# Optimization experiments

Measured on AMD Instinct MI355X. Metric: run time of the kernel, lower is better.

The kernel has to match this reference:

```python
import jax, jax.numpy as jnp
import numpy as np

D_MODEL = 256
NUM_HEADS = 4
EPS = 1e-6


def setup_inputs() -> dict:
    key = jax.random.key(0)
    ks = jax.random.split(key, 9)
    B, T, D = 4, 2048, D_MODEL
    scale = 1.0 / np.sqrt(D)
    inp = {
        "x": jax.random.normal(ks[0], (B, T, D), dtype=jnp.float32),
        "Wq": jax.random.normal(ks[1], (D, D), dtype=jnp.float32) * scale,
        "bq": jnp.zeros((D,), dtype=jnp.float32),
        "Wk": jax.random.normal(ks[2], (D, D), dtype=jnp.float32) * scale,
        "bk": jnp.zeros((D,), dtype=jnp.float32),
        "Wv": jax.random.normal(ks[3], (D, D), dtype=jnp.float32) * scale,
        "bv": jnp.zeros((D,), dtype=jnp.float32),
        "Wo": jax.random.normal(ks[4], (D, D), dtype=jnp.float32) * scale,
        "bo": jnp.zeros((D,), dtype=jnp.float32),
    }
    return inp


def _feature_map(a):
    # F.elu(x) + 1.0
    return jax.nn.elu(a) + 1.0


def reference(x, Wq, bq, Wk, bk, Wv, bv, Wo, bo):
    B, T, D = x.shape
    H = NUM_HEADS
    dh = D // H
    Q = _feature_map((x @ Wq + bq).reshape(B, T, H, dh))
    K = _feature_map((x @ Wk + bk).reshape(B, T, H, dh))
    V = (x @ Wv + bv).reshape(B, T, H, dh)
    # outer-product state: (B,T,H,dh,dh), cumulative over time
    KV = jnp.einsum('bthd,bthm->bthdm', K, V)
    S = jnp.cumsum(KV, axis=1)
    Z = jnp.cumsum(K, axis=1)
    out = jnp.einsum('bthd,bthdm->bthm', Q, S)
    denom = jnp.einsum('bthd,bthd->bth', Q, Z)[..., None] + EPS
    out = (out / denom).reshape(B, T, D)
    return out @ Wo + bo
```

## Files before the change

kernel.cpp:

```cpp
#include <hip/hip_runtime.h>
#include <hip/hip_bf16.h>

#define D_MODEL 256
#define NHEADS 4
#define DHEAD 64
#define BATCH 4
#define TSEQ 2048
#define CHUNK 64
#define NCHUNK (TSEQ / CHUNK)
#define NTOK (BATCH * TSEQ)
#define NBH (BATCH * NHEADS)
#define EPSV 1e-6f
#define LSTRF 68
#define PQ 36

typedef __bf16 bf16x8 __attribute__((ext_vector_type(8)));
typedef float f32x4 __attribute__((ext_vector_type(4)));
typedef unsigned short us8 __attribute__((ext_vector_type(8)));

__device__ __forceinline__ float elu1(float a) {
    return a > 0.0f ? a + 1.0f : __expf(a);
}

__device__ __forceinline__ unsigned short f2bf(float f) {
    __hip_bfloat16 h = __float2bfloat16(f);
    return __builtin_bit_cast(unsigned short, h);
}

__device__ __forceinline__ float bf2f(unsigned short u) {
    return __bfloat162float(__builtin_bit_cast(__hip_bfloat16, u));
}

__device__ __forceinline__ void unpack2(unsigned int u, float& lo, float& hi) {
    lo = __builtin_bit_cast(float, u << 16);
    hi = __builtin_bit_cast(float, u & 0xFFFF0000u);
}

__device__ __forceinline__ bf16x8 frag8(const float* p) {
    const float4 x = *reinterpret_cast<const float4*>(p);
    const float4 y = *reinterpret_cast<const float4*>(p + 4);
    us8 u;
    u[0] = f2bf(x.x); u[1] = f2bf(x.y); u[2] = f2bf(x.z); u[3] = f2bf(x.w);
    u[4] = f2bf(y.x); u[5] = f2bf(y.y); u[6] = f2bf(y.z); u[7] = f2bf(y.w);
    return __builtin_bit_cast(bf16x8, u);
}

__device__ __forceinline__ void gld_lds16(const void* g, void* l) {
    __builtin_amdgcn_global_load_lds(
        (const __attribute__((address_space(1))) void*)g,
        (__attribute__((address_space(3))) void*)l, 16, 0, 0);
}

__global__ __launch_bounds__(256) void convert_kernel(
    const float* __restrict__ x,
    const float* __restrict__ Wq, const float* __restrict__ Wk,
    const float* __restrict__ Wv, const float* __restrict__ Wo,
    unsigned short* __restrict__ xb,
    unsigned short* __restrict__ Wt, unsigned short* __restrict__ Wot)
{
    const int tid = threadIdx.x;
    if (blockIdx.x < NTOK * D_MODEL / 8 / 256) {
        const int i = (blockIdx.x * 256 + tid) * 8;
        const float4 a = *reinterpret_cast<const float4*>(&x[i]);
        const float4 b = *reinterpret_cast<const float4*>(&x[i + 4]);
        ushort4 u0 = { f2bf(a.x), f2bf(a.y), f2bf(a.z), f2bf(a.w) };
        ushort4 u1 = { f2bf(b.x), f2bf(b.y), f2bf(b.z), f2bf(b.w) };
        *reinterpret_cast<ushort4*>(&xb[i]) = u0;
        *reinterpret_cast<ushort4*>(&xb[i + 4]) = u1;
        return;
    }
    __shared__ float Ls[64][65];
    const int bid = blockIdx.x - NTOK * D_MODEL / 8 / 256;
    const int wi = bid >> 4;
    const int ti = bid & 15;
    const int k0 = (ti >> 2) * 64, n0 = (ti & 3) * 64;
    const float* W = wi == 0 ? Wq : wi == 1 ? Wk : wi == 2 ? Wv : Wo;
#pragma unroll
    for (int i = 0; i < 16; ++i) {
        const int idx = i * 256 + tid;
        const int r = idx >> 6, c = idx & 63;
        Ls[r][c] = W[(size_t)(k0 + r) * D_MODEL + n0 + c];
    }
    __syncthreads();
    unsigned short* outp = (wi < 3) ? (Wt + (size_t)(wi * 256 + n0) * D_MODEL + k0)
                                    : (Wot + (size_t)n0 * D_MODEL + k0);
#pragma unroll
    for (int i = 0; i < 16; ++i) {
        const int idx = i * 256 + tid;
        const int rn = idx >> 6, ck = idx & 63;
        outp[(size_t)rn * D_MODEL + ck] = f2bf(Ls[ck][rn]);
    }
}

template<int MODE>
__global__ __launch_bounds__(256) void mfma_gemm_kernel(
    const unsigned short* __restrict__ A,
    const unsigned short* __restrict__ Bt,
    const float* __restrict__ b0, const float* __restrict__ b1,
    const float* __restrict__ b2,
    void* __restrict__ O0, void* __restrict__ O1, void* __restrict__ O2)
{
    __shared__ __align__(16) unsigned short As[64 * 256];
    __shared__ __align__(16) unsigned short Bs[64 * 256];
    const int tid = threadIdx.x;
    const int wave = tid >> 6, lane = tid & 63;
    const int la = lane & 15, q = lane >> 4;

    int mtile, ntile;
    if (MODE == 0) { ntile = blockIdx.x % 12; mtile = blockIdx.x / 12; }
    else           { ntile = blockIdx.x & 3;  mtile = blockIdx.x >> 2; }
    const int m0 = mtile * 64, n0 = ntile * 64;

    const unsigned short* Ab = A  + (size_t)m0 * D_MODEL;
    const unsigned short* Bb = Bt + (size_t)n0 * D_MODEL;

#pragma unroll
    for (int i = 0; i < 8; ++i) {
        const int bslot = i * 256 + wave * 64;
        const int slot = bslot + lane;
        const int m = slot >> 5, s = slot & 31;
        const int g = s ^ (m & 7);
        gld_lds16(Ab + (size_t)m * D_MODEL + g * 8, &As[bslot * 8]);
        gld_lds16(Bb + (size_t)m * D_MODEL + g * 8, &Bs[bslot * 8]);
    }
    __syncthreads();

    f32x4 acc[4];
#pragma unroll
    for (int i = 0; i < 4; ++i) acc[i] = (f32x4){0.f, 0.f, 0.f, 0.f};

#pragma unroll
    for (int kh = 0; kh < 8; ++kh) {
        const int gl = kh * 4 + q;
        const int m = wave * 16 + la;
        const bf16x8 af = *reinterpret_cast<const bf16x8*>(
            &As[m * 256 + ((gl ^ (m & 7)) << 3)]);
#pragma unroll
        for (int ni = 0; ni < 4; ++ni) {
            const int n = ni * 16 + la;
            const bf16x8 bf = *reinterpret_cast<const bf16x8*>(
                &Bs[n * 256 + ((gl ^ (n & 7)) << 3)]);
            acc[ni] = __builtin_amdgcn_mfma_f32_16x16x32_bf16(
                af, bf, acc[ni], 0, 0, 0);
        }
    }

#pragma unroll
    for (int ni = 0; ni < 4; ++ni) {
        const int row = m0 + wave * 16 + q * 4;
        const int col = n0 + ni * 16 + la;
        if (MODE == 0) {
            const int which = col >> 8;
            const int cl = col & 255;
            unsigned short* Out = (unsigned short*)
                (which == 0 ? O0 : which == 1 ? O1 : O2);
            const float* bias = which == 0 ? b0 : which == 1 ? b1 : b2;
            const int act = (which < 2);
            const float bv = bias[cl];
#pragma unroll
            for (int r = 0; r < 4; ++r) {
                float v = acc[ni][r] + bv;
                if (act) v = elu1(v);
                Out[(size_t)(row + r) * D_MODEL + cl] = f2bf(v);
            }
        } else {
            float* Out = (float*)O0;
            const float bv = b0[col];
#pragma unroll
            for (int r = 0; r < 4; ++r)
                Out[(size_t)(row + r) * D_MODEL + col] = acc[ni][r] + bv;
        }
    }
}

__global__ __launch_bounds__(256) void chunksum_kernel(
    const unsigned short* __restrict__ Kb, const unsigned short* __restrict__ Vb,
    unsigned short* __restrict__ Pb16, float* __restrict__ Zc)
{
    __shared__ __align__(16) unsigned int Ktp[DHEAD * PQ];
    __shared__ __align__(16) unsigned int Vtp[DHEAD * PQ];
    const int tid = threadIdx.x;
    const int c  = blockIdx.x % NCHUNK;
    const int bh = blockIdx.x / NCHUNK;
    const int b = bh / NHEADS, h = bh % NHEADS;
    const size_t gbase = ((size_t)(b * TSEQ + c * CHUNK)) * D_MODEL + h * DHEAD;

    {
        const int sp = tid & 31, mg = tid >> 5;
        const int e0 = mg * 8;
        const uint4 k0 = *reinterpret_cast<const uint4*>(
            &Kb[gbase + (size_t)(2 * sp) * D_MODEL + e0]);
        const uint4 k1 = *reinterpret_cast<const uint4*>(
            &Kb[gbase + (size_t)(2 * sp + 1) * D_MODEL + e0]);
        const uint4 v0 = *reinterpret_cast<const uint4*>(
            &Vb[gbase + (size_t)(2 * sp) * D_MODEL + e0]);
        const uint4 v1 = *reinterpret_cast<const uint4*>(
            &Vb[gbase + (size_t)(2 * sp + 1) * D_MODEL + e0]);
        const unsigned short* ke = reinterpret_cast<const unsigned short*>(&k0);
        const unsigned short* ko2 = reinterpret_cast<const unsigned short*>(&k1);
        const unsigned short* ve = reinterpret_cast<const unsigned short*>(&v0);
        const unsigned short* vo = reinterpret_cast<const unsigned short*>(&v1);
#pragma unroll
        for (int j = 0; j < 8; ++j) {
            Ktp[(e0 + j) * PQ + sp] =
                (unsigned int)ke[j] | ((unsigned int)ko2[j] << 16);
            Vtp[(e0 + j) * PQ + sp] =
                (unsigned int)ve[j] | ((unsigned int)vo[j] << 16);
        }
    }
    __syncthreads();

    const int wave = tid >> 6, lane = tid & 63;
    const int la = lane & 15, q = lane >> 4;
    const int wm = (wave >> 1) * 32, wn = (wave & 1) * 32;

    f32x4 acc[2][2];
#pragma unroll
    for (int i = 0; i < 2; ++i)
#pragma unroll
        for (int j = 0; j < 2; ++j) acc[i][j] = (f32x4){0.f, 0.f, 0.f, 0.f};

#pragma unroll
    for (int ks = 0; ks < 2; ++ks) {
        const int ku = ks * 16 + q * 4;
        const bf16x8 a0  = __builtin_bit_cast(bf16x8,
            *reinterpret_cast<const uint4*>(&Vtp[(wm + la) * PQ + ku]));
        const bf16x8 a1  = __builtin_bit_cast(bf16x8,
            *reinterpret_cast<const uint4*>(&Vtp[(wm + 16 + la) * PQ + ku]));
        const bf16x8 bb0 = __builtin_bit_cast(bf16x8,
            *reinterpret_cast<const uint4*>(&Ktp[(wn + la) * PQ + ku]));
        const bf16x8 bb1 = __builtin_bit_cast(bf16x8,
            *reinterpret_cast<const uint4*>(&Ktp[(wn + 16 + la) * PQ + ku]));
        acc[0][0] = __builtin_amdgcn_mfma_f32_16x16x32_bf16(a0, bb0, acc[0][0], 0, 0, 0);
        acc[0][1] = __builtin_amdgcn_mfma_f32_16x16x32_bf16(a0, bb1, acc[0][1], 0, 0, 0);
        acc[1][0] = __builtin_amdgcn_mfma_f32_16x16x32_bf16(a1, bb0, acc[1][0], 0, 0, 0);
        acc[1][1] = __builtin_amdgcn_mfma_f32_16x16x32_bf16(a1, bb1, acc[1][1], 0, 0, 0);
    }

    unsigned short* Pb = Pb16 + (size_t)blockIdx.x * (DHEAD * DHEAD);
#pragma unroll
    for (int mi = 0; mi < 2; ++mi)
#pragma unroll
        for (int ni = 0; ni < 2; ++ni) {
            const int row = wm + mi * 16 + q * 4;
            const int col = wn + ni * 16 + la;
#pragma unroll
            for (int r = 0; r < 4; ++r)
                Pb[(row + r) * DHEAD + col] = f2bf(acc[mi][ni][r]);
        }

    if (tid < DHEAD) {
        float z = 0.f;
        for (int tt = 0; tt < 32; ++tt) {
            float lo, hi;
            unpack2(Ktp[tid * PQ + tt], lo, hi);
            z += lo;
            z += hi;
        }
        Zc[(size_t)blockIdx.x * DHEAD + tid] = z;
    }
}

__global__ __launch_bounds__(256) void prefix_kernel(
    const unsigned short* __restrict__ Pb16, float* __restrict__ Zc,
    unsigned short* __restrict__ Sb)
{
    const int tid = threadIdx.x;
    if (blockIdx.x < NBH * 16) {
        const int bh = blockIdx.x >> 4;
        const int e = ((blockIdx.x & 15) << 8) + tid;
        const size_t base = (size_t)bh * NCHUNK * (DHEAD * DHEAD) + e;
        float v[NCHUNK];
#pragma unroll
        for (int c = 0; c < NCHUNK; ++c)
            v[c] = bf2f(Pb16[base + (size_t)c * (DHEAD * DHEAD)]);
        float s = 0.f;
#pragma unroll
        for (int c = 0; c < NCHUNK; ++c) {
            const float t = v[c];
            Sb[base + (size_t)c * (DHEAD * DHEAD)] = f2bf(s);
            s += t;
        }
    } else {
        const int j = ((int)(blockIdx.x - NBH * 16) << 8) + tid;
        if (j < NBH * DHEAD) {
            const int bh = j >> 6, d = j & 63;
            float v[NCHUNK];
#pragma unroll
            for (int c = 0; c < NCHUNK; ++c) v[c] = Zc[(bh * NCHUNK + c) * DHEAD + d];
            float s = 0.f;
#pragma unroll
            for (int c = 0; c < NCHUNK; ++c) {
                const float t = v[c];
                Zc[(bh * NCHUNK + c) * DHEAD + d] = s;
                s += t;
            }
        }
    }
}

__global__ __launch_bounds__(256) void chunkout_kernel(
    const unsigned short* __restrict__ Qb, const unsigned short* __restrict__ Kb,
    const unsigned short* __restrict__ Vb,
    const unsigned short* __restrict__ Sb, const float* __restrict__ Zx,
    unsigned short* __restrict__ Ob)
{
    __shared__ __align__(16) unsigned int Qp[CHUNK * PQ];
    __shared__ __align__(16) unsigned int Kp[CHUNK * PQ];
    __shared__ __align__(16) unsigned int Vtp[DHEAD * PQ];
    __shared__ __align__(16) float At[CHUNK * LSTRF];
    __shared__ float zsh[DHEAD];
    __shared__ float dnm[CHUNK];

    const int tid = threadIdx.x;
    const int c  = blockIdx.x % NCHUNK;
    const int bh = blockIdx.x / NCHUNK;
    const int b = bh / NHEADS, h = bh % NHEADS;
    const size_t gbase = ((size_t)(b * TSEQ + c * CHUNK)) * D_MODEL + h * DHEAD;
    const unsigned short* Sp = Sb + (size_t)blockIdx.x * (DHEAD * DHEAD);

#pragma unroll
    for (int i = 0; i < 2; ++i) {
        const int idx = i * 256 + tid;
        const int t = idx >> 3, e4 = (idx & 7) * 4;
        const uint4 qv = *reinterpret_cast<const uint4*>(
            &Qb[gbase + (size_t)t * D_MODEL + e4 * 2]);
        const uint4 kv = *reinterpret_cast<const uint4*>(
            &Kb[gbase + (size_t)t * D_MODEL + e4 * 2]);
        *reinterpret_cast<uint4*>(&Qp[t * PQ + e4]) = qv;
        *reinterpret_cast<uint4*>(&Kp[t * PQ + e4]) = kv;
    }
    {
        const int sp = tid & 31, mg = tid >> 5;
        const int m0 = mg * 8;
        const uint4 v0 = *reinterpret_cast<const uint4*>(
            &Vb[gbase + (size_t)(2 * sp) * D_MODEL + m0]);
        const uint4 v1 = *reinterpret_cast<const uint4*>(
            &Vb[gbase + (size_t)(2 * sp + 1) * D_MODEL + m0]);
        const unsigned short* ev = reinterpret_cast<const unsigned short*>(&v0);
        const unsigned short* ov = reinterpret_cast<const unsigned short*>(&v1);
#pragma unroll
        for (int j = 0; j < 8; ++j)
            Vtp[(m0 + j) * PQ + sp] =
                (unsigned int)ev[j] | ((unsigned int)ov[j] << 16);
    }
    if (tid < DHEAD)
        zsh[tid] = Zx[((size_t)bh * NCHUNK + c) * DHEAD + tid];
    __syncthreads();

    const int wave = tid >> 6, lane = tid & 63;
    const int la = lane & 15, q = lane >> 4;
    const int wt = (wave >> 1) * 32, wn = (wave & 1) * 32;

    f32x4 acc[2][2];
#pragma unroll
    for (int i = 0; i < 2; ++i)
#pragma unroll
        for (int j = 0; j < 2; ++j) acc[i][j] = (f32x4){0.f, 0.f, 0.f, 0.f};
#pragma unroll
    for (int ks = 0; ks < 2; ++ks) {
        const int ku = ks * 16 + q * 4;
        const bf16x8 a0  = __builtin_bit_cast(bf16x8,
            *reinterpret_cast<const uint4*>(&Qp[(wt + la) * PQ + ku]));
        const bf16x8 a1  = __builtin_bit_cast(bf16x8,
            *reinterpret_cast<const uint4*>(&Qp[(wt + 16 + la) * PQ + ku]));
        const bf16x8 bb0 = __builtin_bit_cast(bf16x8,
            *reinterpret_cast<const uint4*>(&Kp[(wn + la) * PQ + ku]));
        const bf16x8 bb1 = __builtin_bit_cast(bf16x8,
            *reinterpret_cast<const uint4*>(&Kp[(wn + 16 + la) * PQ + ku]));
        acc[0][0] = __builtin_amdgcn_mfma_f32_16x16x32_bf16(a0, bb0, acc[0][0], 0, 0, 0);
        acc[0][1] = __builtin_amdgcn_mfma_f32_16x16x32_bf16(a0, bb1, acc[0][1], 0, 0, 0);
        acc[1][0] = __builtin_amdgcn_mfma_f32_16x16x32_bf16(a1, bb0, acc[1][0], 0, 0, 0);
        acc[1][1] = __builtin_amdgcn_mfma_f32_16x16x32_bf16(a1, bb1, acc[1][1], 0, 0, 0);
    }
#pragma unroll
    for (int mi = 0; mi < 2; ++mi)
#pragma unroll
        for (int ni = 0; ni < 2; ++ni) {
            const int t0 = wt + mi * 16 + q * 4;
            const int s  = wn + ni * 16 + la;
#pragma unroll
            for (int r = 0; r < 4; ++r)
                At[(t0 + r) * LSTRF + s] = (s <= t0 + r) ? acc[mi][ni][r] : 0.f;
        }
    __syncthreads();

    if (tid < CHUNK) {
        float dv = 0.f;
        for (int s = 0; s < CHUNK; ++s) dv += At[tid * LSTRF + s];
        for (int dd = 0; dd < 32; ++dd) {
            float lo, hi;
            unpack2(Qp[tid * PQ + dd], lo, hi);
            dv = fmaf(lo, zsh[2 * dd], dv);
            dv = fmaf(hi, zsh[2 * dd + 1], dv);
        }
        dnm[tid] = dv + EPSV;
    }
    __syncthreads();

    f32x4 o[2][2];
#pragma unroll
    for (int i = 0; i < 2; ++i)
#pragma unroll
        for (int j = 0; j < 2; ++j) o[i][j] = (f32x4){0.f, 0.f, 0.f, 0.f};
#pragma unroll
    for (int ks = 0; ks < 2; ++ks) {
        const int ku = ks * 16 + q * 4;
        const int ko = ks * 32 + q * 8;
        const bf16x8 a0  = __builtin_bit_cast(bf16x8,
            *reinterpret_cast<const uint4*>(&Qp[(wt + la) * PQ + ku]));
        const bf16x8 a1  = __builtin_bit_cast(bf16x8,
            *reinterpret_cast<const uint4*>(&Qp[(wt + 16 + la) * PQ + ku]));
        const bf16x8 bb0 = __builtin_bit_cast(bf16x8,
            *reinterpret_cast<const uint4*>(&Sp[(wn + la) * DHEAD + ko]));
        const bf16x8 bb1 = __builtin_bit_cast(bf16x8,
            *reinterpret_cast<const uint4*>(&Sp[(wn + 16 + la) * DHEAD + ko]));
        o[0][0] = __builtin_amdgcn_mfma_f32_16x16x32_bf16(a0, bb0, o[0][0], 0, 0, 0);
        o[0][1] = __builtin_amdgcn_mfma_f32_16x16x32_bf16(a0, bb1, o[0][1], 0, 0, 0);
        o[1][0] = __builtin_amdgcn_mfma_f32_16x16x32_bf16(a1, bb0, o[1][0], 0, 0, 0);
        o[1][1] = __builtin_amdgcn_mfma_f32_16x16x32_bf16(a1, bb1, o[1][1], 0, 0, 0);
    }
#pragma unroll
    for (int ks = 0; ks < 2; ++ks) {
        const int ku = ks * 16 + q * 4;
        const int ko = ks * 32 + q * 8;
        const bf16x8 a0  = frag8(&At[(wt + la) * LSTRF + ko]);
        const bf16x8 a1  = frag8(&At[(wt + 16 + la) * LSTRF + ko]);
        const bf16x8 bb0 = __builtin_bit_cast(bf16x8,
            *reinterpret_cast<const uint4*>(&Vtp[(wn + la) * PQ + ku]));
        const bf16x8 bb1 = __builtin_bit_cast(bf16x8,
            *reinterpret_cast<const uint4*>(&Vtp[(wn + 16 + la) * PQ + ku]));
        o[0][0] = __builtin_amdgcn_mfma_f32_16x16x32_bf16(a0, bb0, o[0][0], 0, 0, 0);
        o[0][1] = __builtin_amdgcn_mfma_f32_16x16x32_bf16(a0, bb1, o[0][1], 0, 0, 0);
        o[1][0] = __builtin_amdgcn_mfma_f32_16x16x32_bf16(a1, bb0, o[1][0], 0, 0, 0);
        o[1][1] = __builtin_amdgcn_mfma_f32_16x16x32_bf16(a1, bb1, o[1][1], 0, 0, 0);
    }

#pragma unroll
    for (int mi = 0; mi < 2; ++mi)
#pragma unroll
        for (int ni = 0; ni < 2; ++ni) {
            const int t0 = wt + mi * 16 + q * 4;
            const int m  = wn + ni * 16 + la;
#pragma unroll
            for (int r = 0; r < 4; ++r) {
                const float v = o[mi][ni][r] / dnm[t0 + r];
                Ob[gbase + (size_t)(t0 + r) * D_MODEL + m] = f2bf(v);
            }
        }
}

extern "C" void kernel_launch(void* const* d_in, const int* in_sizes, int n_in,
                              void* d_out, int out_size, void* d_ws, size_t ws_size,
                              hipStream_t stream)
{
    const float* x  = (const float*)d_in[0];
    const float* Wq = (const float*)d_in[1];
    const float* bq = (const float*)d_in[2];
    const float* Wk = (const float*)d_in[3];
    const float* bk = (const float*)d_in[4];
    const float* Wv = (const float*)d_in[5];
    const float* bv = (const float*)d_in[6];
    const float* Wo = (const float*)d_in[7];
    const float* bo = (const float*)d_in[8];
    float* out = (float*)d_out;

    const size_t NE = (size_t)NTOK * D_MODEL;
    const size_t PE = (size_t)NBH * NCHUNK * DHEAD * DHEAD;
    unsigned short* xb   = (unsigned short*)d_ws;
    unsigned short* Wt   = xb + NE;
    unsigned short* Wot  = Wt + 768 * 256;
    unsigned short* Qb   = Wot + 256 * 256;
    unsigned short* Kb   = Qb + NE;
    unsigned short* Vb   = Kb + NE;
    unsigned short* Ob   = Vb + NE;
    unsigned short* Sb   = Ob + NE;
    unsigned short* Pb16 = Sb + PE;
    float* Z = (float*)(Pb16 + PE);

    convert_kernel<<<NTOK * D_MODEL / 8 / 256 + 64, 256, 0, stream>>>(
        x, Wq, Wk, Wv, Wo, xb, Wt, Wot);
    mfma_gemm_kernel<0><<<(NTOK / 64) * 12, 256, 0, stream>>>(
        xb, Wt, bq, bk, bv, Qb, Kb, Vb);
    chunksum_kernel<<<NBH * NCHUNK, 256, 0, stream>>>(Kb, Vb, Pb16, Z);
    prefix_kernel<<<NBH * 16 + 4, 256, 0, stream>>>(Pb16, Z, Sb);
    chunkout_kernel<<<NBH * NCHUNK, 256, 0, stream>>>(Qb, Kb, Vb, Sb, Z, Ob);
    mfma_gemm_kernel<1><<<(NTOK / 64) * 4, 256, 0, stream>>>(
        Ob, Wot, bo, nullptr, nullptr, out, nullptr, nullptr);
}
```

Before: 106.4 us.

## Fuse fp32-to-bf16 conversion into GEMMs and fold chunk prefix scan into chunkout

Drops the separate convert kernel: the QKV and output GEMMs now load fp32 x and weights directly, converting to bf16 and transposing into swizzled LDS. Drops the prefix kernel: each chunkout block sums all earlier chunk states and key sums on the fly from global memory into register fragments. This removes two launches and the intermediate xb/Wt/Sb buffers. In exchange, weights are read with strided scalar loads, and later chunks re-read up to 31 prefix states, which adds quadratic redundant global traffic and load imbalance across blocks.

```diff
diff --git a/kernel.cpp b/kernel.cpp
--- a/kernel.cpp
+++ b/kernel.cpp
@@ -45,60 +45,27 @@
     return __builtin_bit_cast(bf16x8, u);
 }
 
+__device__ __forceinline__ bf16x8 pack8(const float* p) {
+    us8 u;
+#pragma unroll
+    for (int j = 0; j < 8; ++j) u[j] = f2bf(p[j]);
+    return __builtin_bit_cast(bf16x8, u);
+}
+
 __device__ __forceinline__ void gld_lds16(const void* g, void* l) {
     __builtin_amdgcn_global_load_lds(
         (const __attribute__((address_space(1))) void*)g,
         (__attribute__((address_space(3))) void*)l, 16, 0, 0);
 }
 
-__global__ __launch_bounds__(256) void convert_kernel(
+__global__ __launch_bounds__(256) void qkv_kernel(
     const float* __restrict__ x,
     const float* __restrict__ Wq, const float* __restrict__ Wk,
-    const float* __restrict__ Wv, const float* __restrict__ Wo,
-    unsigned short* __restrict__ xb,
-    unsigned short* __restrict__ Wt, unsigned short* __restrict__ Wot)
-{
-    const int tid = threadIdx.x;
-    if (blockIdx.x < NTOK * D_MODEL / 8 / 256) {
-        const int i = (blockIdx.x * 256 + tid) * 8;
-        const float4 a = *reinterpret_cast<const float4*>(&x[i]);
-        const float4 b = *reinterpret_cast<const float4*>(&x[i + 4]);
-        ushort4 u0 = { f2bf(a.x), f2bf(a.y), f2bf(a.z), f2bf(a.w) };
-        ushort4 u1 = { f2bf(b.x), f2bf(b.y), f2bf(b.z), f2bf(b.w) };
-        *reinterpret_cast<ushort4*>(&xb[i]) = u0;
-        *reinterpret_cast<ushort4*>(&xb[i + 4]) = u1;
-        return;
-    }
-    __shared__ float Ls[64][65];
-    const int bid = blockIdx.x - NTOK * D_MODEL / 8 / 256;
-    const int wi = bid >> 4;
-    const int ti = bid & 15;
-    const int k0 = (ti >> 2) * 64, n0 = (ti & 3) * 64;
-    const float* W = wi == 0 ? Wq : wi == 1 ? Wk : wi == 2 ? Wv : Wo;
-#pragma unroll
-    for (int i = 0; i < 16; ++i) {
-        const int idx = i * 256 + tid;
-        const int r = idx >> 6, c = idx & 63;
-        Ls[r][c] = W[(size_t)(k0 + r) * D_MODEL + n0 + c];
-    }
-    __syncthreads();
-    unsigned short* outp = (wi < 3) ? (Wt + (size_t)(wi * 256 + n0) * D_MODEL + k0)
-                                    : (Wot + (size_t)n0 * D_MODEL + k0);
-#pragma unroll
-    for (int i = 0; i < 16; ++i) {
-        const int idx = i * 256 + tid;
-        const int rn = idx >> 6, ck = idx & 63;
-        outp[(size_t)rn * D_MODEL + ck] = f2bf(Ls[ck][rn]);
-    }
-}
-
-template<int MODE>
-__global__ __launch_bounds__(256) void mfma_gemm_kernel(
-    const unsigned short* __restrict__ A,
-    const unsigned short* __restrict__ Bt,
-    const float* __restrict__ b0, const float* __restrict__ b1,
-    const float* __restrict__ b2,
-    void* __restrict__ O0, void* __restrict__ O1, void* __restrict__ O2)
+    const float* __restrict__ Wv,
+    const float* __restrict__ bq, const float* __restrict__ bk,
+    const float* __restrict__ bv,
+    unsigned short* __restrict__ Qb, unsigned short* __restrict__ Kb,
+    unsigned short* __restrict__ Vb)
 {
     __shared__ __align__(16) unsigned short As[64 * 256];
     __shared__ __align__(16) unsigned short Bs[64 * 256];
@@ -106,13 +73,90 @@
     const int wave = tid >> 6, lane = tid & 63;
     const int la = lane & 15, q = lane >> 4;
 
-    int mtile, ntile;
-    if (MODE == 0) { ntile = blockIdx.x % 12; mtile = blockIdx.x / 12; }
-    else           { ntile = blockIdx.x & 3;  mtile = blockIdx.x >> 2; }
+    const int ntile = blockIdx.x % 12, mtile = blockIdx.x / 12;
+    const int m0 = mtile * 64;
+    const int which = ntile >> 2;
+    const int wcol0 = (ntile & 3) * 64;
+    const float* W    = which == 0 ? Wq : which == 1 ? Wk : Wv;
+    const float* bias = which == 0 ? bq : which == 1 ? bk : bv;
+    unsigned short* Out = which == 0 ? Qb : which == 1 ? Kb : Vb;
+    const int act = (which < 2);
+
+#pragma unroll
+    for (int i = 0; i < 8; ++i) {
+        const int task = i * 256 + tid;
+        const int m = task >> 5, g = task & 31;
+        const float* src = &x[(size_t)(m0 + m) * D_MODEL + g * 8];
+        const float4 a = *reinterpret_cast<const float4*>(src);
+        const float4 b = *reinterpret_cast<const float4*>(src + 4);
+        us8 u;
+        u[0] = f2bf(a.x); u[1] = f2bf(a.y); u[2] = f2bf(a.z); u[3] = f2bf(a.w);
+        u[4] = f2bf(b.x); u[5] = f2bf(b.y); u[6] = f2bf(b.z); u[7] = f2bf(b.w);
+        *reinterpret_cast<us8*>(&As[m * 256 + ((g ^ (m & 7)) << 3)]) = u;
+    }
+#pragma unroll
+    for (int i = 0; i < 8; ++i) {
+        const int task = i * 256 + tid;
+        const int n = task & 63, g = (task >> 6) + i * 4 * 0 + (i * 4) * 0;
+        const int gg = i * 4 + (task >> 6 & 3);
+        const int k0 = gg * 8;
+        us8 u;
+#pragma unroll
+        for (int j = 0; j < 8; ++j)
+            u[j] = f2bf(W[(size_t)(k0 + j) * D_MODEL + wcol0 + n]);
+        *reinterpret_cast<us8*>(&Bs[n * 256 + ((gg ^ (n & 7)) << 3)]) = u;
+        (void)g;
+    }
+    __syncthreads();
+
+    f32x4 acc[4];
+#pragma unroll
+    for (int i = 0; i < 4; ++i) acc[i] = (f32x4){0.f, 0.f, 0.f, 0.f};
+
+#pragma unroll
+    for (int kh = 0; kh < 8; ++kh) {
+        const int gl = kh * 4 + q;
+        const int m = wave * 16 + la;
+        const bf16x8 af = *reinterpret_cast<const bf16x8*>(
+            &As[m * 256 + ((gl ^ (m & 7)) << 3)]);
+#pragma unroll
+        for (int ni = 0; ni < 4; ++ni) {
+            const int n = ni * 16 + la;
+            const bf16x8 bf = *reinterpret_cast<const bf16x8*>(
+                &Bs[n * 256 + ((gl ^ (n & 7)) << 3)]);
+            acc[ni] = __builtin_amdgcn_mfma_f32_16x16x32_bf16(
+                af, bf, acc[ni], 0, 0, 0);
+        }
+    }
+
+#pragma unroll
+    for (int ni = 0; ni < 4; ++ni) {
+        const int row = m0 + wave * 16 + q * 4;
+        const int cl = wcol0 + ni * 16 + la;
+        const float bv2 = bias[cl];
+#pragma unroll
+        for (int r = 0; r < 4; ++r) {
+            float v = acc[ni][r] + bv2;
+            if (act) v = elu1(v);
+            Out[(size_t)(row + r) * D_MODEL + cl] = f2bf(v);
+        }
+    }
+}
+
+__global__ __launch_bounds__(256) void ogemm_kernel(
+    const unsigned short* __restrict__ Ob, const float* __restrict__ Wo,
+    const float* __restrict__ bo, float* __restrict__ out)
+{
+    __shared__ __align__(16) unsigned short As[64 * 256];
+    __shared__ __align__(16) unsigned short Bs[64 * 256];
+    const int tid = threadIdx.x;
+    const int wave = tid >> 6, lane = tid & 63;
+    const int la = lane & 15, q = lane >> 4;
+
+    const int ntile = blockIdx.x & 3, mtile = blockIdx.x >> 2;
     const int m0 = mtile * 64, n0 = ntile * 64;
 
-    const unsigned short* Ab = A  + (size_t)m0 * D_MODEL;
-    const unsigned short* Bb = Bt + (size_t)n0 * D_MODEL;
+    const unsigned short* Ab = Ob + (size_t)m0 * D_MODEL;
 
 #pragma unroll
     for (int i = 0; i < 8; ++i) {
@@ -121,7 +165,18 @@
         const int m = slot >> 5, s = slot & 31;
         const int g = s ^ (m & 7);
         gld_lds16(Ab + (size_t)m * D_MODEL + g * 8, &As[bslot * 8]);
-        gld_lds16(Bb + (size_t)m * D_MODEL + g * 8, &Bs[bslot * 8]);
+    }
+#pragma unroll
+    for (int i = 0; i < 8; ++i) {
+        const int task = i * 256 + tid;
+        const int n = task & 63;
+        const int gg = i * 4 + (task >> 6 & 3);
+        const int k0 = gg * 8;
+        us8 u;
+#pragma unroll
+        for (int j = 0; j < 8; ++j)
+            u[j] = f2bf(Wo[(size_t)(k0 + j) * D_MODEL + n0 + n]);
+        *reinterpret_cast<us8*>(&Bs[n * 256 + ((gg ^ (n & 7)) << 3)]) = u;
     }
     __syncthreads();
 
@@ -149,27 +204,10 @@
     for (int ni = 0; ni < 4; ++ni) {
         const int row = m0 + wave * 16 + q * 4;
         const int col = n0 + ni * 16 + la;
-        if (MODE == 0) {
-            const int which = col >> 8;
-            const int cl = col & 255;
-            unsigned short* Out = (unsigned short*)
-                (which == 0 ? O0 : which == 1 ? O1 : O2);
-            const float* bias = which == 0 ? b0 : which == 1 ? b1 : b2;
-            const int act = (which < 2);
-            const float bv = bias[cl];
-#pragma unroll
-            for (int r = 0; r < 4; ++r) {
-                float v = acc[ni][r] + bv;
-                if (act) v = elu1(v);
-                Out[(size_t)(row + r) * D_MODEL + cl] = f2bf(v);
-            }
-        } else {
-            float* Out = (float*)O0;
-            const float bv = b0[col];
-#pragma unroll
-            for (int r = 0; r < 4; ++r)
-                Out[(size_t)(row + r) * D_MODEL + col] = acc[ni][r] + bv;
-        }
+        const float bv2 = bo[col];
+#pragma unroll
+        for (int r = 0; r < 4; ++r)
+            out[(size_t)(row + r) * D_MODEL + col] = acc[ni][r] + bv2;
     }
 }
 
@@ -261,48 +299,10 @@
     }
 }
 
-__global__ __launch_bounds__(256) void prefix_kernel(
-    const unsigned short* __restrict__ Pb16, float* __restrict__ Zc,
-    unsigned short* __restrict__ Sb)
-{
-    const int tid = threadIdx.x;
-    if (blockIdx.x < NBH * 16) {
-        const int bh = blockIdx.x >> 4;
-        const int e = ((blockIdx.x & 15) << 8) + tid;
-        const size_t base = (size_t)bh * NCHUNK * (DHEAD * DHEAD) + e;
-        float v[NCHUNK];
-#pragma unroll
-        for (int c = 0; c < NCHUNK; ++c)
-            v[c] = bf2f(Pb16[base + (size_t)c * (DHEAD * DHEAD)]);
-        float s = 0.f;
-#pragma unroll
-        for (int c = 0; c < NCHUNK; ++c) {
-            const float t = v[c];
-            Sb[base + (size_t)c * (DHEAD * DHEAD)] = f2bf(s);
-            s += t;
-        }
-    } else {
-        const int j = ((int)(blockIdx.x - NBH * 16) << 8) + tid;
-        if (j < NBH * DHEAD) {
-            const int bh = j >> 6, d = j & 63;
-            float v[NCHUNK];
-#pragma unroll
-            for (int c = 0; c < NCHUNK; ++c) v[c] = Zc[(bh * NCHUNK + c) * DHEAD + d];
-            float s = 0.f;
-#pragma unroll
-            for (int c = 0; c < NCHUNK; ++c) {
-                const float t = v[c];
-                Zc[(bh * NCHUNK + c) * DHEAD + d] = s;
-                s += t;
-            }
-        }
-    }
-}
-
 __global__ __launch_bounds__(256) void chunkout_kernel(
     const unsigned short* __restrict__ Qb, const unsigned short* __restrict__ Kb,
     const unsigned short* __restrict__ Vb,
-    const unsigned short* __restrict__ Sb, const float* __restrict__ Zx,
+    const unsigned short* __restrict__ Pb16, const float* __restrict__ Zc,
     unsigned short* __restrict__ Ob)
 {
     __shared__ __align__(16) unsigned int Qp[CHUNK * PQ];
@@ -317,7 +317,10 @@
     const int bh = blockIdx.x / NCHUNK;
     const int b = bh / NHEADS, h = bh % NHEADS;
     const size_t gbase = ((size_t)(b * TSEQ + c * CHUNK)) * D_MODEL + h * DHEAD;
-    const unsigned short* Sp = Sb + (size_t)blockIdx.x * (DHEAD * DHEAD);
+
+    const int wave = tid >> 6, lane = tid & 63;
+    const int la = lane & 15, q = lane >> 4;
+    const int wt = (wave >> 1) * 32, wn = (wave & 1) * 32;
 
 #pragma unroll
     for (int i = 0; i < 2; ++i) {
@@ -344,13 +347,54 @@
             Vtp[(m0 + j) * PQ + sp] =
                 (unsigned int)ev[j] | ((unsigned int)ov[j] << 16);
     }
-    if (tid < DHEAD)
-        zsh[tid] = Zx[((size_t)bh * NCHUNK + c) * DHEAD + tid];
+    if (tid < DHEAD) {
+        float zv = 0.f;
+        for (int cc = 0; cc < c; ++cc)
+            zv += Zc[((size_t)bh * NCHUNK + cc) * DHEAD + tid];
+        zsh[tid] = zv;
+    }
+
+    float sacc[2][2][8];
+#pragma unroll
+    for (int ri = 0; ri < 2; ++ri)
+#pragma unroll
+        for (int ks = 0; ks < 2; ++ks)
+#pragma unroll
+            for (int j = 0; j < 8; ++j) sacc[ri][ks][j] = 0.f;
+    {
+        const unsigned short* Pbase =
+            Pb16 + (size_t)bh * NCHUNK * (DHEAD * DHEAD);
+        const int r0 = wn + la, r1 = wn + 16 + la;
+        for (int cc = 0; cc < c; ++cc) {
+            const unsigned short* Pc = Pbase + (size_t)cc * (DHEAD * DHEAD);
+#pragma unroll
+            for (int ri = 0; ri < 2; ++ri) {
+                const int row = ri ? r1 : r0;
+#pragma unroll
+                for (int ks = 0; ks < 2; ++ks) {
+                    const int ko = ks * 32 + q * 8;
+                    const uint4 v = *reinterpret_cast<const uint4*>(
+                        &Pc[row * DHEAD + ko]);
+                    const unsigned int* w = reinterpret_cast<const unsigned int*>(&v);
+#pragma unroll
+                    for (int d = 0; d < 4; ++d) {
+                        float lo, hi;
+                        unpack2(w[d], lo, hi);
+                        sacc[ri][ks][2 * d]     += lo;
+                        sacc[ri][ks][2 * d + 1] += hi;
+                    }
+                }
+            }
+        }
+    }
+    bf16x8 sfrag[2][2];
+#pragma unroll
+    for (int ri = 0; ri < 2; ++ri)
+#pragma unroll
+        for (int ks = 0; ks < 2; ++ks)
+            sfrag[ri][ks] = pack8(sacc[ri][ks]);
+
     __syncthreads();
-
-    const int wave = tid >> 6, lane = tid & 63;
-    const int la = lane & 15, q = lane >> 4;
-    const int wt = (wave >> 1) * 32, wn = (wave & 1) * 32;
 
     f32x4 acc[2][2];
 #pragma unroll
@@ -406,15 +450,12 @@
 #pragma unroll
     for (int ks = 0; ks < 2; ++ks) {
         const int ku = ks * 16 + q * 4;
-        const int ko = ks * 32 + q * 8;
         const bf16x8 a0  = __builtin_bit_cast(bf16x8,
             *reinterpret_cast<const uint4*>(&Qp[(wt + la) * PQ + ku]));
         const bf16x8 a1  = __builtin_bit_cast(bf16x8,
             *reinterpret_cast<const uint4*>(&Qp[(wt + 16 + la) * PQ + ku]));
-        const bf16x8 bb0 = __builtin_bit_cast(bf16x8,
-            *reinterpret_cast<const uint4*>(&Sp[(wn + la) * DHEAD + ko]));
-        const bf16x8 bb1 = __builtin_bit_cast(bf16x8,
-            *reinterpret_cast<const uint4*>(&Sp[(wn + 16 + la) * DHEAD + ko]));
+        const bf16x8 bb0 = sfrag[0][ks];
+        const bf16x8 bb1 = sfrag[1][ks];
         o[0][0] = __builtin_amdgcn_mfma_f32_16x16x32_bf16(a0, bb0, o[0][0], 0, 0, 0);
         o[0][1] = __builtin_amdgcn_mfma_f32_16x16x32_bf16(a0, bb1, o[0][1], 0, 0, 0);
         o[1][0] = __builtin_amdgcn_mfma_f32_16x16x32_bf16(a1, bb0, o[1][0], 0, 0, 0);
@@ -467,24 +508,16 @@
 
     const size_t NE = (size_t)NTOK * D_MODEL;
     const size_t PE = (size_t)NBH * NCHUNK * DHEAD * DHEAD;
-    unsigned short* xb   = (unsigned short*)d_ws;
-    unsigned short* Wt   = xb + NE;
-    unsigned short* Wot  = Wt + 768 * 256;
-    unsigned short* Qb   = Wot + 256 * 256;
+    unsigned short* Qb   = (unsigned short*)d_ws;
     unsigned short* Kb   = Qb + NE;
     unsigned short* Vb   = Kb + NE;
     unsigned short* Ob   = Vb + NE;
-    unsigned short* Sb   = Ob + NE;
-    unsigned short* Pb16 = Sb + PE;
+    unsigned short* Pb16 = Ob + NE;
     float* Z = (float*)(Pb16 + PE);
 
-    convert_kernel<<<NTOK * D_MODEL / 8 / 256 + 64, 256, 0, stream>>>(
-        x, Wq, Wk, Wv, Wo, xb, Wt, Wot);
-    mfma_gemm_kernel<0><<<(NTOK / 64) * 12, 256, 0, stream>>>(
-        xb, Wt, bq, bk, bv, Qb, Kb, Vb);
+    qkv_kernel<<<(NTOK / 64) * 12, 256, 0, stream>>>(
+        x, Wq, Wk, Wv, bq, bk, bv, Qb, Kb, Vb);
     chunksum_kernel<<<NBH * NCHUNK, 256, 0, stream>>>(Kb, Vb, Pb16, Z);
-    prefix_kernel<<<NBH * 16 + 4, 256, 0, stream>>>(Pb16, Z, Sb);
-    chunkout_kernel<<<NBH * NCHUNK, 256, 0, stream>>>(Qb, Kb, Vb, Sb, Z, Ob);
-    mfma_gemm_kernel<1><<<(NTOK / 64) * 4, 256, 0, stream>>>(
-        Ob, Wot, bo, nullptr, nullptr, out, nullptr, nullptr);
-}
+    chunkout_kernel<<<NBH * NCHUNK, 256, 0, stream>>>(Qb, Kb, Vb, Pb16, Z, Ob);
+    ogemm_kernel<<<(NTOK / 64) * 4, 256, 0, stream>>>(Ob, Wo, bo, out);
+}
```

Measured after the change: 133.0 us. 1.25x slower.

## Fuse QKV projection GEMM with per-chunk KV outer-product summation

Applied to the files above, without the earlier changes.

Merges the QKV projection GEMM and the chunk-sum kernel into one kernel. Each block handles one (batch, head, chunk), computes its Q, K and V tiles, and writes K and V transposed into shared memory so it can form the chunk KV product and Z sum without reading K and V back from global memory. This removes a launch and a global round trip of K and V. In exchange the grid shrinks to 512 blocks, each doing three sequential GEMM passes with weight tiles staged in halves and extra barriers, which may lower parallelism. The output GEMM is split into its own non-templated kernel.

```diff
diff --git a/kernel.cpp b/kernel.cpp
--- a/kernel.cpp
+++ b/kernel.cpp
@@ -92,28 +92,29 @@
     }
 }
 
-template<int MODE>
-__global__ __launch_bounds__(256) void mfma_gemm_kernel(
-    const unsigned short* __restrict__ A,
-    const unsigned short* __restrict__ Bt,
-    const float* __restrict__ b0, const float* __restrict__ b1,
-    const float* __restrict__ b2,
-    void* __restrict__ O0, void* __restrict__ O1, void* __restrict__ O2)
+__global__ __launch_bounds__(256) void qkvcs_kernel(
+    const unsigned short* __restrict__ xb, const unsigned short* __restrict__ Wt,
+    const float* __restrict__ bq, const float* __restrict__ bk,
+    const float* __restrict__ bv,
+    unsigned short* __restrict__ Qb, unsigned short* __restrict__ Kb,
+    unsigned short* __restrict__ Vb,
+    unsigned short* __restrict__ Pb16, float* __restrict__ Zc)
 {
     __shared__ __align__(16) unsigned short As[64 * 256];
-    __shared__ __align__(16) unsigned short Bs[64 * 256];
+    __shared__ __align__(16) unsigned short Bs[64 * 128];
+    __shared__ __align__(16) unsigned int Ktp[DHEAD * PQ];
+    __shared__ __align__(16) unsigned int Vtp[DHEAD * PQ];
+
     const int tid = threadIdx.x;
     const int wave = tid >> 6, lane = tid & 63;
     const int la = lane & 15, q = lane >> 4;
-
-    int mtile, ntile;
-    if (MODE == 0) { ntile = blockIdx.x % 12; mtile = blockIdx.x / 12; }
-    else           { ntile = blockIdx.x & 3;  mtile = blockIdx.x >> 2; }
-    const int m0 = mtile * 64, n0 = ntile * 64;
-
-    const unsigned short* Ab = A  + (size_t)m0 * D_MODEL;
-    const unsigned short* Bb = Bt + (size_t)n0 * D_MODEL;
-
+    const int c  = blockIdx.x % NCHUNK;
+    const int bh = blockIdx.x / NCHUNK;
+    const int b = bh / NHEADS, h = bh % NHEADS;
+    const int m0 = b * TSEQ + c * CHUNK;
+    const size_t gbase = (size_t)m0 * D_MODEL + h * DHEAD;
+
+    const unsigned short* Ab = xb + (size_t)m0 * D_MODEL;
 #pragma unroll
     for (int i = 0; i < 8; ++i) {
         const int bslot = i * 256 + wave * 64;
@@ -121,104 +122,86 @@
         const int m = slot >> 5, s = slot & 31;
         const int g = s ^ (m & 7);
         gld_lds16(Ab + (size_t)m * D_MODEL + g * 8, &As[bslot * 8]);
-        gld_lds16(Bb + (size_t)m * D_MODEL + g * 8, &Bs[bslot * 8]);
+    }
+
+#pragma unroll
+    for (int w = 0; w < 3; ++w) {
+        const float* bias = w == 0 ? bq : w == 1 ? bk : bv;
+        unsigned short* Out = w == 0 ? Qb : w == 1 ? Kb : Vb;
+        const unsigned short* Wb = Wt + (size_t)(w * 256 + h * 64) * D_MODEL;
+
+        f32x4 acc[4];
+#pragma unroll
+        for (int i = 0; i < 4; ++i) acc[i] = (f32x4){0.f, 0.f, 0.f, 0.f};
+
+#pragma unroll
+        for (int half = 0; half < 2; ++half) {
+#pragma unroll
+            for (int i = 0; i < 4; ++i) {
+                const int bslot = i * 256 + wave * 64;
+                const int slot = bslot + lane;
+                const int n = slot >> 4, s = slot & 15;
+                const int g = s ^ (n & 7);
+                gld_lds16(Wb + (size_t)n * D_MODEL + half * 128 + g * 8,
+                          &Bs[bslot * 8]);
+            }
+            __syncthreads();
+#pragma unroll
+            for (int kh = 0; kh < 4; ++kh) {
+                const int glA = half * 16 + kh * 4 + q;
+                const int glB = kh * 4 + q;
+                const int m = wave * 16 + la;
+                const bf16x8 af = *reinterpret_cast<const bf16x8*>(
+                    &As[m * 256 + ((glA ^ (m & 7)) << 3)]);
+#pragma unroll
+                for (int ni = 0; ni < 4; ++ni) {
+                    const int n = ni * 16 + la;
+                    const bf16x8 bf = *reinterpret_cast<const bf16x8*>(
+                        &Bs[n * 128 + ((glB ^ (n & 7)) << 3)]);
+                    acc[ni] = __builtin_amdgcn_mfma_f32_16x16x32_bf16(
+                        af, bf, acc[ni], 0, 0, 0);
+                }
+            }
+            __syncthreads();
+        }
+
+#pragma unroll
+        for (int ni = 0; ni < 4; ++ni) {
+            const int cl = ni * 16 + la;
+            const float bv2 = bias[h * 64 + cl];
+            float vv[4];
+#pragma unroll
+            for (int r = 0; r < 4; ++r) {
+                float v = acc[ni][r] + bv2;
+                if (w < 2) v = elu1(v);
+                vv[r] = v;
+                const int t = wave * 16 + q * 4 + r;
+                Out[gbase + (size_t)t * D_MODEL + cl] = f2bf(v);
+            }
+            if (w == 1) {
+#pragma unroll
+                for (int pr = 0; pr < 2; ++pr)
+                    Ktp[cl * PQ + wave * 8 + q * 2 + pr] =
+                        (unsigned int)f2bf(vv[2 * pr]) |
+                        ((unsigned int)f2bf(vv[2 * pr + 1]) << 16);
+            } else if (w == 2) {
+#pragma unroll
+                for (int pr = 0; pr < 2; ++pr)
+                    Vtp[cl * PQ + wave * 8 + q * 2 + pr] =
+                        (unsigned int)f2bf(vv[2 * pr]) |
+                        ((unsigned int)f2bf(vv[2 * pr + 1]) << 16);
+            }
+        }
     }
     __syncthreads();
 
-    f32x4 acc[4];
-#pragma unroll
-    for (int i = 0; i < 4; ++i) acc[i] = (f32x4){0.f, 0.f, 0.f, 0.f};
-
-#pragma unroll
-    for (int kh = 0; kh < 8; ++kh) {
-        const int gl = kh * 4 + q;
-        const int m = wave * 16 + la;
-        const bf16x8 af = *reinterpret_cast<const bf16x8*>(
-            &As[m * 256 + ((gl ^ (m & 7)) << 3)]);
-#pragma unroll
-        for (int ni = 0; ni < 4; ++ni) {
-            const int n = ni * 16 + la;
-            const bf16x8 bf = *reinterpret_cast<const bf16x8*>(
-                &Bs[n * 256 + ((gl ^ (n & 7)) << 3)]);
-            acc[ni] = __builtin_amdgcn_mfma_f32_16x16x32_bf16(
-                af, bf, acc[ni], 0, 0, 0);
-        }
-    }
-
-#pragma unroll
-    for (int ni = 0; ni < 4; ++ni) {
-        const int row = m0 + wave * 16 + q * 4;
-        const int col = n0 + ni * 16 + la;
-        if (MODE == 0) {
-            const int which = col >> 8;
-            const int cl = col & 255;
-            unsigned short* Out = (unsigned short*)
-                (which == 0 ? O0 : which == 1 ? O1 : O2);
-            const float* bias = which == 0 ? b0 : which == 1 ? b1 : b2;
-            const int act = (which < 2);
-            const float bv = bias[cl];
-#pragma unroll
-            for (int r = 0; r < 4; ++r) {
-                float v = acc[ni][r] + bv;
-                if (act) v = elu1(v);
-                Out[(size_t)(row + r) * D_MODEL + cl] = f2bf(v);
-            }
-        } else {
-            float* Out = (float*)O0;
-            const float bv = b0[col];
-#pragma unroll
-            for (int r = 0; r < 4; ++r)
-                Out[(size_t)(row + r) * D_MODEL + col] = acc[ni][r] + bv;
-        }
-    }
-}
-
-__global__ __launch_bounds__(256) void chunksum_kernel(
-    const unsigned short* __restrict__ Kb, const unsigned short* __restrict__ Vb,
-    unsigned short* __restrict__ Pb16, float* __restrict__ Zc)
-{
-    __shared__ __align__(16) unsigned int Ktp[DHEAD * PQ];
-    __shared__ __align__(16) unsigned int Vtp[DHEAD * PQ];
-    const int tid = threadIdx.x;
-    const int c  = blockIdx.x % NCHUNK;
-    const int bh = blockIdx.x / NCHUNK;
-    const int b = bh / NHEADS, h = bh % NHEADS;
-    const size_t gbase = ((size_t)(b * TSEQ + c * CHUNK)) * D_MODEL + h * DHEAD;
-
-    {
-        const int sp = tid & 31, mg = tid >> 5;
-        const int e0 = mg * 8;
-        const uint4 k0 = *reinterpret_cast<const uint4*>(
-            &Kb[gbase + (size_t)(2 * sp) * D_MODEL + e0]);
-        const uint4 k1 = *reinterpret_cast<const uint4*>(
-            &Kb[gbase + (size_t)(2 * sp + 1) * D_MODEL + e0]);
-        const uint4 v0 = *reinterpret_cast<const uint4*>(
-            &Vb[gbase + (size_t)(2 * sp) * D_MODEL + e0]);
-        const uint4 v1 = *reinterpret_cast<const uint4*>(
-            &Vb[gbase + (size_t)(2 * sp + 1) * D_MODEL + e0]);
-        const unsigned short* ke = reinterpret_cast<const unsigned short*>(&k0);
-        const unsigned short* ko2 = reinterpret_cast<const unsigned short*>(&k1);
-        const unsigned short* ve = reinterpret_cast<const unsigned short*>(&v0);
-        const unsigned short* vo = reinterpret_cast<const unsigned short*>(&v1);
-#pragma unroll
-        for (int j = 0; j < 8; ++j) {
-            Ktp[(e0 + j) * PQ + sp] =
-                (unsigned int)ke[j] | ((unsigned int)ko2[j] << 16);
-            Vtp[(e0 + j) * PQ + sp] =
-                (unsigned int)ve[j] | ((unsigned int)vo[j] << 16);
-        }
-    }
-    __syncthreads();
-
-    const int wave = tid >> 6, lane = tid & 63;
-    const int la = lane & 15, q = lane >> 4;
     const int wm = (wave >> 1) * 32, wn = (wave & 1) * 32;
 
-    f32x4 acc[2][2];
+    f32x4 pacc[2][2];
 #pragma unroll
     for (int i = 0; i < 2; ++i)
 #pragma unroll
-        for (int j = 0; j < 2; ++j) acc[i][j] = (f32x4){0.f, 0.f, 0.f, 0.f};
+        for (int j = 0; j < 2; ++j) pacc[i][j] = (f32x4){0.f, 0.f, 0.f, 0.f};
 
 #pragma unroll
     for (int ks = 0; ks < 2; ++ks) {
@@ -231,10 +214,10 @@
             *reinterpret_cast<const uint4*>(&Ktp[(wn + la) * PQ + ku]));
         const bf16x8 bb1 = __builtin_bit_cast(bf16x8,
             *reinterpret_cast<const uint4*>(&Ktp[(wn + 16 + la) * PQ + ku]));
-        acc[0][0] = __builtin_amdgcn_mfma_f32_16x16x32_bf16(a0, bb0, acc[0][0], 0, 0, 0);
-        acc[0][1] = __builtin_amdgcn_mfma_f32_16x16x32_bf16(a0, bb1, acc[0][1], 0, 0, 0);
-        acc[1][0] = __builtin_amdgcn_mfma_f32_16x16x32_bf16(a1, bb0, acc[1][0], 0, 0, 0);
-        acc[1][1] = __builtin_amdgcn_mfma_f32_16x16x32_bf16(a1, bb1, acc[1][1], 0, 0, 0);
+        pacc[0][0] = __builtin_amdgcn_mfma_f32_16x16x32_bf16(a0, bb0, pacc[0][0], 0, 0, 0);
+        pacc[0][1] = __builtin_amdgcn_mfma_f32_16x16x32_bf16(a0, bb1, pacc[0][1], 0, 0, 0);
+        pacc[1][0] = __builtin_amdgcn_mfma_f32_16x16x32_bf16(a1, bb0, pacc[1][0], 0, 0, 0);
+        pacc[1][1] = __builtin_amdgcn_mfma_f32_16x16x32_bf16(a1, bb1, pacc[1][1], 0, 0, 0);
     }
 
     unsigned short* Pb = Pb16 + (size_t)blockIdx.x * (DHEAD * DHEAD);
@@ -246,7 +229,7 @@
             const int col = wn + ni * 16 + la;
 #pragma unroll
             for (int r = 0; r < 4; ++r)
-                Pb[(row + r) * DHEAD + col] = f2bf(acc[mi][ni][r]);
+                Pb[(row + r) * DHEAD + col] = f2bf(pacc[mi][ni][r]);
         }
 
     if (tid < DHEAD) {
@@ -450,6 +433,65 @@
         }
 }
 
+__global__ __launch_bounds__(256) void ogemm_kernel(
+    const unsigned short* __restrict__ A,
+    const unsigned short* __restrict__ Bt,
+    const float* __restrict__ b0, float* __restrict__ out)
+{
+    __shared__ __align__(16) unsigned short As[64 * 256];
+    __shared__ __align__(16) unsigned short Bs[64 * 256];
+    const int tid = threadIdx.x;
+    const int wave = tid >> 6, lane = tid & 63;
+    const int la = lane & 15, q = lane >> 4;
+
+    const int ntile = blockIdx.x & 3, mtile = blockIdx.x >> 2;
+    const int m0 = mtile * 64, n0 = ntile * 64;
+
+    const unsigned short* Ab = A  + (size_t)m0 * D_MODEL;
+    const unsigned short* Bb = Bt + (size_t)n0 * D_MODEL;
+
+#pragma unroll
+    for (int i = 0; i < 8; ++i) {
+        const int bslot = i * 256 + wave * 64;
+        const int slot = bslot + lane;
+        const int m = slot >> 5, s = slot & 31;
+        const int g = s ^ (m & 7);
+        gld_lds16(Ab + (size_t)m * D_MODEL + g * 8, &As[bslot * 8]);
+        gld_lds16(Bb + (size_t)m * D_MODEL + g * 8, &Bs[bslot * 8]);
+    }
+    __syncthreads();
+
+    f32x4 acc[4];
+#pragma unroll
+    for (int i = 0; i < 4; ++i) acc[i] = (f32x4){0.f, 0.f, 0.f, 0.f};
+
+#pragma unroll
+    for (int kh = 0; kh < 8; ++kh) {
+        const int gl = kh * 4 + q;
+        const int m = wave * 16 + la;
+        const bf16x8 af = *reinterpret_cast<const bf16x8*>(
+            &As[m * 256 + ((gl ^ (m & 7)) << 3)]);
+#pragma unroll
+        for (int ni = 0; ni < 4; ++ni) {
+            const int n = ni * 16 + la;
+            const bf16x8 bf = *reinterpret_cast<const bf16x8*>(
+                &Bs[n * 256 + ((gl ^ (n & 7)) << 3)]);
+            acc[ni] = __builtin_amdgcn_mfma_f32_16x16x32_bf16(
+                af, bf, acc[ni], 0, 0, 0);
+        }
+    }
+
+#pragma unroll
+    for (int ni = 0; ni < 4; ++ni) {
+        const int row = m0 + wave * 16 + q * 4;
+        const int col = n0 + ni * 16 + la;
+        const float bv2 = b0[col];
+#pragma unroll
+        for (int r = 0; r < 4; ++r)
+            out[(size_t)(row + r) * D_MODEL + col] = acc[ni][r] + bv2;
+    }
+}
+
 extern "C" void kernel_launch(void* const* d_in, const int* in_sizes, int n_in,
                               void* d_out, int out_size, void* d_ws, size_t ws_size,
                               hipStream_t stream)
@@ -480,11 +522,9 @@
 
     convert_kernel<<<NTOK * D_MODEL / 8 / 256 + 64, 256, 0, stream>>>(
         x, Wq, Wk, Wv, Wo, xb, Wt, Wot);
-    mfma_gemm_kernel<0><<<(NTOK / 64) * 12, 256, 0, stream>>>(
-        xb, Wt, bq, bk, bv, Qb, Kb, Vb);
-    chunksum_kernel<<<NBH * NCHUNK, 256, 0, stream>>>(Kb, Vb, Pb16, Z);
+    qkvcs_kernel<<<NBH * NCHUNK, 256, 0, stream>>>(
+        xb, Wt, bq, bk, bv, Qb, Kb, Vb, Pb16, Z);
     prefix_kernel<<<NBH * 16 + 4, 256, 0, stream>>>(Pb16, Z, Sb);
     chunkout_kernel<<<NBH * NCHUNK, 256, 0, stream>>>(Qb, Kb, Vb, Sb, Z, Ob);
-    mfma_gemm_kernel<1><<<(NTOK / 64) * 4, 256, 0, stream>>>(
-        Ob, Wot, bo, nullptr, nullptr, out, nullptr, nullptr);
-}
+    ogemm_kernel<<<(NTOK / 64) * 4, 256, 0, stream>>>(Ob, Wot, bo, out);
+}
```

After: 104.6 us. Within noise of the previous version (-1.6%).
